# Kernel tuning notes

Measured on AMD Instinct MI355X. Metric: run time of the kernel, lower is better.

The kernel has to match this reference:

```python
import jax, jax.numpy as jnp
import numpy as np

B, S, XDIM, YDIM = 64, 1024, 256, 128


def setup_inputs() -> dict:
    key = jax.random.key(0)
    ks = jax.random.split(key, 7)
    q = jax.random.normal(ks[0], (B, S, XDIM), dtype=jnp.float32)
    # Linear weights in torch layout [out, in]; biases [out]
    sc = 1.0 / np.sqrt(XDIM)
    Wq = jax.random.normal(ks[1], (YDIM, XDIM), dtype=jnp.float32) * sc
    Wk = jax.random.normal(ks[2], (YDIM, XDIM), dtype=jnp.float32) * sc
    Wv = jax.random.normal(ks[3], (YDIM, XDIM), dtype=jnp.float32) * sc
    bq = jax.random.normal(ks[4], (YDIM,), dtype=jnp.float32) * sc
    bk = jax.random.normal(ks[5], (YDIM,), dtype=jnp.float32) * sc
    bv = jax.random.normal(ks[6], (YDIM,), dtype=jnp.float32) * sc
    return {"q": q, "Wq": Wq, "bq": bq, "Wk": Wk, "bk": bk, "Wv": Wv, "bv": bv}


def reference(q, Wq, bq, Wk, bk, Wv, bv):
    # Q, K, V projections: [B, S, YDIM]
    Q = jnp.einsum('bsx,yx->bsy', q, Wq) + bq
    K = jnp.einsum('bsx,yx->bsy', q, Wk) + bk
    V = jnp.einsum('bsx,yx->bsy', q, Wv) + bv
    scale = jnp.float32(np.sqrt(YDIM))
    # scores [B, S_q, S_k]; softmax over the QUERY axis (dim=-2), non-standard
    scores = jnp.einsum('bqd,bkd->bqk', Q, K) / scale
    attn = jax.nn.softmax(scores, axis=-2)
    out = jnp.einsum('bqk,bkd->bqd', attn, V)  # [B, S, YDIM]
    # flat=True: max over dim=-2 -> [B, YDIM]
    return jnp.max(out, axis=-2)
```

## Files before the change

### kernel.cpp

```cpp
#include <hip/hip_runtime.h>

typedef __bf16 bf16;
typedef __attribute__((ext_vector_type(8))) __bf16 bf16x8;
typedef __attribute__((ext_vector_type(4))) __bf16 bf16x4;
typedef __attribute__((ext_vector_type(4))) float  f32x4;

static __device__ __forceinline__ f32x4 mfma16(bf16x8 a, bf16x8 b, f32x4 c) {
  return __builtin_amdgcn_mfma_f32_16x16x32_bf16(a, b, c, 0, 0, 0);
}
static __device__ __forceinline__ float fexp2(float x) {
  return __builtin_amdgcn_exp2f(x);
}

#define EXP_C1 (1.4426950408889634f / 11.313708498984760f)

typedef const __attribute__((address_space(1))) unsigned int gas_u32;
typedef __attribute__((address_space(3))) unsigned int las_u32;
#define GLDS16(gp, lp) __builtin_amdgcn_global_load_lds((gas_u32*)(gp), (las_u32*)(lp), 16, 0, 0)

#define DMA_FENCE() __asm__ volatile("s_waitcnt vmcnt(0)" ::: "memory")


__global__ __launch_bounds__(256) void k_prep(
    const float* __restrict__ Wq, const float* __restrict__ Wk,
    const float* __restrict__ Wv, bf16* __restrict__ Wc)
{
  int id = blockIdx.x * 256 + threadIdx.x;
  int proj = id >> 12, r = id & 4095;
  int g = r >> 7, n = r & 127;
  const float* W = proj == 0 ? Wq : proj == 1 ? Wk : Wv;
  const float4* src = (const float4*)(W + n * 256 + g * 8);
  float4 a = src[0], b = src[1];
  bf16x8 o = { (bf16)a.x, (bf16)a.y, (bf16)a.z, (bf16)a.w,
               (bf16)b.x, (bf16)b.y, (bf16)b.z, (bf16)b.w };
  *(bf16x8*)(Wc + (size_t)proj * 32768 + g * 1024 + n * 8) = o;
}

__global__ __launch_bounds__(256, 4) void k_qkv(
    const float* __restrict__ q, const bf16* __restrict__ Wc,
    const float* __restrict__ bq, const float* __restrict__ bk, const float* __restrict__ bv,
    bf16* __restrict__ Qb, bf16* __restrict__ Kb, bf16* __restrict__ VT)
{
  __shared__ bf16 Al[32 * 520];

  const int tid = threadIdx.x, lane = tid & 63, wave = tid >> 6;
  const int ln = lane & 15, quad = lane >> 4;
  const int wc = wave;
  const int m0 = blockIdx.x * 64;

  {
    const float* src = q + (size_t)m0 * 256;
    for (int it = 0; it < 16; ++it) {
      int f = it * 1024 + tid * 4;
      int r = f >> 8, c = f & 255;
      float4 v = *(const float4*)(src + f);
      bf16x4 o = { (bf16)v.x, (bf16)v.y, (bf16)v.z, (bf16)v.w };
      *(bf16x4*)&Al[(c >> 3) * 520 + r * 8 + (c & 7)] = o;
    }
  }
  __syncthreads();

  const int b = m0 >> 10, st = (m0 & 1023) >> 7, s_off = m0 & 64;
  const size_t tbase = ((size_t)b * 8 + st) * 16384;

  for (int p = 0; p < 3; ++p) {
    const bf16* W = Wc + (size_t)p * 32768;
    const float* bias = p == 0 ? bq : p == 1 ? bk : bv;
    if (p < 2) {
      f32x4 acc[2][4] = {};
      for (int kk = 0; kk < 8; ++kk) {
        int g = kk * 4 + quad;
        bf16x8 ax[4], bw[2];
        for (int t = 0; t < 4; ++t)
          ax[t] = *(const bf16x8*)&Al[g * 520 + (t * 16 + ln) * 8];
        for (int t = 0; t < 2; ++t)
          bw[t] = *(const bf16x8*)(W + g * 1024 + (wc * 32 + t * 16 + ln) * 8);
        for (int i = 0; i < 2; ++i)
          for (int j = 0; j < 4; ++j)
            acc[i][j] = mfma16(bw[i], ax[j], acc[i][j]);
      }
      bf16* dst = (p == 0 ? Qb : Kb) + tbase;
      for (int i = 0; i < 2; ++i) {
        float4 b4 = *(const float4*)&bias[wc * 32 + i * 16 + quad * 4];
        int gd = wc * 4 + i * 2 + (quad >> 1);
        int e0 = (quad & 1) * 4;
        for (int j = 0; j < 4; ++j) {
          int s = s_off + j * 16 + ln;
          bf16x4 o = { (bf16)(acc[i][j][0] + b4.x), (bf16)(acc[i][j][1] + b4.y),
                       (bf16)(acc[i][j][2] + b4.z), (bf16)(acc[i][j][3] + b4.w) };
          *(bf16x4*)&dst[(size_t)gd * 1024 + (size_t)s * 8 + e0] = o;
        }
      }
    } else {
      f32x4 acc[4][2] = {};
      for (int kk = 0; kk < 8; ++kk) {
        int g = kk * 4 + quad;
        bf16x8 ax[4], bw[2];
        for (int t = 0; t < 4; ++t)
          ax[t] = *(const bf16x8*)&Al[g * 520 + (t * 16 + ln) * 8];
        for (int t = 0; t < 2; ++t)
          bw[t] = *(const bf16x8*)(W + g * 1024 + (wc * 32 + t * 16 + ln) * 8);
        for (int i = 0; i < 4; ++i)
          for (int j = 0; j < 2; ++j)
            acc[i][j] = mfma16(ax[i], bw[j], acc[i][j]);
      }
      bf16* dst = VT + tbase;
      for (int j = 0; j < 2; ++j) {
        int d = wc * 32 + j * 16 + ln;
        float bb = bias[d];
        for (int i = 0; i < 4; ++i) {
          int s0 = s_off + i * 16 + quad * 4;
          int G  = (s0 >> 5) * 4 + ((s0 & 15) >> 2);
          int e0 = (s0 & 16) >> 2;
          bf16x4 o = { (bf16)(acc[i][j][0] + bb), (bf16)(acc[i][j][1] + bb),
                       (bf16)(acc[i][j][2] + bb), (bf16)(acc[i][j][3] + bb) };
          *(bf16x4*)&dst[(size_t)G * 1024 + (size_t)d * 8 + e0] = o;
        }
      }
    }
  }
}

__global__ __launch_bounds__(256, 2) void k_stats(
    const bf16* __restrict__ Qb, const bf16* __restrict__ Kb, float* __restrict__ inv)
{
  __shared__ char Qbuf[2][32768];
  const int b = blockIdx.x, kt = blockIdx.y;
  const int tid = threadIdx.x, lane = tid & 63, wave = tid >> 6;
  const int ln = lane & 15, quad = lane >> 4;

  const bf16* ktile = Kb + ((size_t)b * 8 + kt) * 16384;
  bf16x8 ak[2][4];
  for (int i = 0; i < 2; ++i)
    for (int kk = 0; kk < 4; ++kk)
      ak[i][kk] = *(const bf16x8*)(ktile + (kk * 4 + quad) * 1024 + (wave * 32 + i * 16 + ln) * 8);

  const char* qb_b = (const char*)(Qb + (size_t)b * 8 * 16384);
  for (int c = 0; c < 8; ++c)
    GLDS16(qb_b + (wave * 8 + c) * 1024 + lane * 16, &Qbuf[0][(wave * 8 + c) * 1024]);

  f32x4 csum[2] = {};
  for (int qt = 0; qt < 8; ++qt) {
    DMA_FENCE();
    __syncthreads();
    if (qt < 7)
      for (int c = 0; c < 8; ++c)
        GLDS16(qb_b + (size_t)(qt + 1) * 32768 + (wave * 8 + c) * 1024 + lane * 16,
               &Qbuf[(qt + 1) & 1][(wave * 8 + c) * 1024]);
    const char* Ql = Qbuf[qt & 1];
    for (int jq = 0; jq < 8; ++jq) {
      f32x4 s0 = {}, s1 = {};
      for (int kk = 0; kk < 4; ++kk) {
        bf16x8 bqf = *(const bf16x8*)(Ql + ((kk * 4 + quad) * 2 + (jq >> 2)) * 1024
                                         + ((jq * 16 + ln) & 63) * 16);
        s0 = mfma16(ak[0][kk], bqf, s0);
        s1 = mfma16(ak[1][kk], bqf, s1);
      }
      for (int rr = 0; rr < 4; ++rr) {
        csum[0][rr] += fexp2(s0[rr] * EXP_C1);
        csum[1][rr] += fexp2(s1[rr] * EXP_C1);
      }
    }
  }
  for (int i = 0; i < 2; ++i)
    for (int rr = 0; rr < 4; ++rr) {
      float v = csum[i][rr];
      v += __shfl_xor(v, 1, 64); v += __shfl_xor(v, 2, 64);
      v += __shfl_xor(v, 4, 64); v += __shfl_xor(v, 8, 64);
      csum[i][rr] = v;
    }
  if (ln == 0) {
    float* dst = inv + (size_t)b * 1024 + kt * 128 + wave * 32 + quad * 4;
    for (int i = 0; i < 2; ++i)
      for (int rr = 0; rr < 4; ++rr)
        dst[i * 16 + rr] = 1.0f / csum[i][rr];
  }
}

__global__ __launch_bounds__(256, 2) void k_attn(
    const bf16* __restrict__ Qb, const bf16* __restrict__ Kb, const bf16* __restrict__ VT,
    const float* __restrict__ inv, float* __restrict__ Opart)
{
  __shared__ char buf[2][32768];
  __shared__ float invl[1024];
  __shared__ float redm[4][128];

  const int b = blockIdx.x, qt = blockIdx.y;
  const int tid = threadIdx.x, lane = tid & 63, wave = tid >> 6;
  const int ln = lane & 15, quad = lane >> 4;

  *(float4*)&invl[tid * 4] = *(const float4*)(inv + (size_t)b * 1024 + tid * 4);

  const bf16* qtile = Qb + ((size_t)b * 8 + qt) * 16384;
  bf16x8 bq_[2][4];
  for (int j = 0; j < 2; ++j)
    for (int kk = 0; kk < 4; ++kk)
      bq_[j][kk] = *(const bf16x8*)(qtile + (kk * 4 + quad) * 1024 + (wave * 32 + j * 16 + ln) * 8);

  const char* kb_b = (const char*)(Kb + (size_t)b * 8 * 16384);
  const char* vt_b = (const char*)(VT + (size_t)b * 8 * 16384);

#define DMA_TILE(t) do {                                                         \
    const char* ksrc = kb_b + (size_t)((t) >> 1) * 32768 + ((t) & 1) * 1024;     \
    const char* vsrc = vt_b + (size_t)((t) >> 1) * 32768 + ((t) & 1) * 16384;    \
    char* d_ = buf[(t) & 1];                                                     \
    for (int c = 0; c < 4; ++c) {                                                \
      int ch = wave * 4 + c;                                                     \
      GLDS16(ksrc + ch * 2048 + lane * 16, d_ + ch * 1024);                      \
      GLDS16(vsrc + (ch >> 1) * 2048 + (ch & 1) * 1024 + lane * 16,              \
             d_ + 16384 + ch * 1024);                                            \
    }                                                                            \
  } while (0)

  f32x4 oacc[2][8] = {};
  DMA_TILE(0);

  for (int t = 0; t < 16; ++t) {
    DMA_FENCE();
    __syncthreads();
    if (t < 15) DMA_TILE(t + 1);
    const char* Kl = buf[t & 1];
    const char* Vl = buf[t & 1] + 16384;

    f32x4 sacc[4][2] = {};
    for (int kk = 0; kk < 4; ++kk) {
      bf16x8 ak[4];
      for (int i = 0; i < 4; ++i)
        ak[i] = *(const bf16x8*)(Kl + (kk * 4 + quad) * 1024 + (i * 16 + ln) * 16);
      for (int i = 0; i < 4; ++i)
        for (int j = 0; j < 2; ++j)
          sacc[i][j] = mfma16(ak[i], bq_[j][kk], sacc[i][j]);
    }
    bf16x8 pf[2][2];
    for (int s = 0; s < 2; ++s) {
      float4 iv0 = *(float4*)&invl[t * 64 + (2 * s) * 16 + quad * 4];
      float4 iv1 = *(float4*)&invl[t * 64 + (2 * s + 1) * 16 + quad * 4];
      for (int j = 0; j < 2; ++j) {
        f32x4 lo = sacc[2 * s][j], hi = sacc[2 * s + 1][j];
        pf[j][s] = bf16x8{
          (bf16)(fexp2(lo[0] * EXP_C1) * iv0.x), (bf16)(fexp2(lo[1] * EXP_C1) * iv0.y),
          (bf16)(fexp2(lo[2] * EXP_C1) * iv0.z), (bf16)(fexp2(lo[3] * EXP_C1) * iv0.w),
          (bf16)(fexp2(hi[0] * EXP_C1) * iv1.x), (bf16)(fexp2(hi[1] * EXP_C1) * iv1.y),
          (bf16)(fexp2(hi[2] * EXP_C1) * iv1.z), (bf16)(fexp2(hi[3] * EXP_C1) * iv1.w) };
      }
    }
    for (int s = 0; s < 2; ++s)
      for (int j2 = 0; j2 < 8; ++j2) {
        bf16x8 bv_ = *(const bf16x8*)(Vl + ((s * 4 + quad) * 2 + (j2 >> 2)) * 1024
                                         + ((j2 * 16 + ln) & 63) * 16);
        oacc[0][j2] = mfma16(pf[0][s], bv_, oacc[0][j2]);
        oacc[1][j2] = mfma16(pf[1][s], bv_, oacc[1][j2]);
      }
  }

  for (int j2 = 0; j2 < 8; ++j2) {
    float m = -3.4e38f;
    for (int j = 0; j < 2; ++j)
      for (int rr = 0; rr < 4; ++rr)
        m = fmaxf(m, oacc[j][j2][rr]);
    m = fmaxf(m, __shfl_xor(m, 16, 64));
    m = fmaxf(m, __shfl_xor(m, 32, 64));
    if (lane < 16) redm[wave][j2 * 16 + ln] = m;
  }
  __syncthreads();
  if (tid < 128)
    Opart[((size_t)b * 8 + qt) * 128 + tid] =
      fmaxf(fmaxf(redm[0][tid], redm[1][tid]), fmaxf(redm[2][tid], redm[3][tid]));
}

__global__ __launch_bounds__(256) void k_final(
    const float* __restrict__ Opart, float* __restrict__ out)
{
  int t = blockIdx.x * 256 + threadIdx.x;
  int b = t >> 7, d = t & 127;
  const float* p = Opart + (size_t)b * 1024 + d;
  float m = p[0];
  for (int i = 1; i < 8; ++i) m = fmaxf(m, p[(size_t)i * 128]);
  out[t] = m;
}

extern "C" void kernel_launch(void* const* d_in, const int* in_sizes, int n_in,
                              void* d_out, int out_size, void* d_ws, size_t ws_size,
                              hipStream_t stream) {
  const float* q  = (const float*)d_in[0];
  const float* Wq = (const float*)d_in[1];
  const float* bq = (const float*)d_in[2];
  const float* Wk = (const float*)d_in[3];
  const float* bk = (const float*)d_in[4];
  const float* Wv = (const float*)d_in[5];
  const float* bv = (const float*)d_in[6];
  float* out = (float*)d_out;

  char* ws = (char*)d_ws;
  bf16*  Qb    = (bf16*)(ws);
  bf16*  Kb    = (bf16*)(ws + (16u << 20));
  bf16*  VT    = (bf16*)(ws + (32u << 20));
  float* inv   = (float*)(ws + (48u << 20));
  float* Opart = (float*)(ws + (48u << 20) + (512u << 10));
  bf16*  Wc    = (bf16*)(ws + (49u << 20));

  k_prep <<<48,           256, 0, stream>>>(Wq, Wk, Wv, Wc);
  k_qkv  <<<dim3(1024),   256, 0, stream>>>(q, Wc, bq, bk, bv, Qb, Kb, VT);
  k_stats<<<dim3(64, 8),  256, 0, stream>>>(Qb, Kb, inv);
  k_attn <<<dim3(64, 8),  256, 0, stream>>>(Qb, Kb, VT, inv, Opart);
  k_final<<<32, 256, 0, stream>>>(Opart, out);
}
```

Measured before the change: 92.57 us.

## Halve per-block tile in stats and attention kernels to double grid size

The stats and attention kernels now give each block 64 key or query rows instead of 128. Each wave owns 16 rows, and the K/V and Q streaming tiles shrink to 32 or 64 rows, so the grid grows from 512 to 1024 blocks and LDS per block halves, allowing 4 blocks per CU. The goal is more blocks and occupancy to hide latency on a GPU with many CUs. The cost is that each block reloads the full Q (stats) or K/V (attention) stream for half the work, doubling that global/L2 traffic and the barrier count per unit of work, and k_final now reduces 16 partials.

```diff
diff --git a/kernel.cpp b/kernel.cpp
--- a/kernel.cpp
+++ b/kernel.cpp
@@ -121,67 +121,64 @@
   }
 }
 
-__global__ __launch_bounds__(256, 2) void k_stats(
+__global__ __launch_bounds__(256, 4) void k_stats(
     const bf16* __restrict__ Qb, const bf16* __restrict__ Kb, float* __restrict__ inv)
 {
-  __shared__ char Qbuf[2][32768];
+  __shared__ char Qbuf[2][16384];
   const int b = blockIdx.x, kt = blockIdx.y;
   const int tid = threadIdx.x, lane = tid & 63, wave = tid >> 6;
   const int ln = lane & 15, quad = lane >> 4;
 
-  const bf16* ktile = Kb + ((size_t)b * 8 + kt) * 16384;
-  bf16x8 ak[2][4];
-  for (int i = 0; i < 2; ++i)
-    for (int kk = 0; kk < 4; ++kk)
-      ak[i][kk] = *(const bf16x8*)(ktile + (kk * 4 + quad) * 1024 + (wave * 32 + i * 16 + ln) * 8);
+  const bf16* ktile = Kb + ((size_t)b * 8 + (kt >> 1)) * 16384;
+  const int krow = (kt & 1) * 64 + wave * 16 + ln;
+  bf16x8 ak[4];
+  for (int kk = 0; kk < 4; ++kk)
+    ak[kk] = *(const bf16x8*)(ktile + (kk * 4 + quad) * 1024 + krow * 8);
 
   const char* qb_b = (const char*)(Qb + (size_t)b * 8 * 16384);
-  for (int c = 0; c < 8; ++c)
-    GLDS16(qb_b + (wave * 8 + c) * 1024 + lane * 16, &Qbuf[0][(wave * 8 + c) * 1024]);
-
-  f32x4 csum[2] = {};
-  for (int qt = 0; qt < 8; ++qt) {
+#define QDMA(c) do {                                                            \
+    char* d_ = Qbuf[(c) & 1];                                                   \
+    for (int cc = 0; cc < 4; ++cc) {                                            \
+      int ck = wave * 4 + cc;                                                   \
+      GLDS16(qb_b + (size_t)((c) >> 1) * 32768 + ck * 2048 + ((c) & 1) * 1024   \
+                  + lane * 16, d_ + ck * 1024);                                 \
+    }                                                                           \
+  } while (0)
+
+  QDMA(0);
+  f32x4 csum = {};
+  for (int c = 0; c < 16; ++c) {
     DMA_FENCE();
     __syncthreads();
-    if (qt < 7)
-      for (int c = 0; c < 8; ++c)
-        GLDS16(qb_b + (size_t)(qt + 1) * 32768 + (wave * 8 + c) * 1024 + lane * 16,
-               &Qbuf[(qt + 1) & 1][(wave * 8 + c) * 1024]);
-    const char* Ql = Qbuf[qt & 1];
-    for (int jq = 0; jq < 8; ++jq) {
-      f32x4 s0 = {}, s1 = {};
+    if (c < 15) QDMA(c + 1);
+    const char* Ql = Qbuf[c & 1];
+    for (int jq = 0; jq < 4; ++jq) {
+      f32x4 s = {};
       for (int kk = 0; kk < 4; ++kk) {
-        bf16x8 bqf = *(const bf16x8*)(Ql + ((kk * 4 + quad) * 2 + (jq >> 2)) * 1024
-                                         + ((jq * 16 + ln) & 63) * 16);
-        s0 = mfma16(ak[0][kk], bqf, s0);
-        s1 = mfma16(ak[1][kk], bqf, s1);
-      }
-      for (int rr = 0; rr < 4; ++rr) {
-        csum[0][rr] += fexp2(s0[rr] * EXP_C1);
-        csum[1][rr] += fexp2(s1[rr] * EXP_C1);
-      }
-    }
-  }
-  for (int i = 0; i < 2; ++i)
-    for (int rr = 0; rr < 4; ++rr) {
-      float v = csum[i][rr];
-      v += __shfl_xor(v, 1, 64); v += __shfl_xor(v, 2, 64);
-      v += __shfl_xor(v, 4, 64); v += __shfl_xor(v, 8, 64);
-      csum[i][rr] = v;
-    }
+        bf16x8 bqf = *(const bf16x8*)(Ql + (kk * 4 + quad) * 1024 + (jq * 16 + ln) * 16);
+        s = mfma16(ak[kk], bqf, s);
+      }
+      for (int rr = 0; rr < 4; ++rr) csum[rr] += fexp2(s[rr] * EXP_C1);
+    }
+  }
+  for (int rr = 0; rr < 4; ++rr) {
+    float v = csum[rr];
+    v += __shfl_xor(v, 1, 64); v += __shfl_xor(v, 2, 64);
+    v += __shfl_xor(v, 4, 64); v += __shfl_xor(v, 8, 64);
+    csum[rr] = v;
+  }
   if (ln == 0) {
-    float* dst = inv + (size_t)b * 1024 + kt * 128 + wave * 32 + quad * 4;
-    for (int i = 0; i < 2; ++i)
-      for (int rr = 0; rr < 4; ++rr)
-        dst[i * 16 + rr] = 1.0f / csum[i][rr];
-  }
-}
-
-__global__ __launch_bounds__(256, 2) void k_attn(
+    float* dst = inv + (size_t)b * 1024 + kt * 64 + wave * 16 + quad * 4;
+    for (int rr = 0; rr < 4; ++rr) dst[rr] = 1.0f / csum[rr];
+  }
+#undef QDMA
+}
+
+__global__ __launch_bounds__(256, 4) void k_attn(
     const bf16* __restrict__ Qb, const bf16* __restrict__ Kb, const bf16* __restrict__ VT,
     const float* __restrict__ inv, float* __restrict__ Opart)
 {
-  __shared__ char buf[2][32768];
+  __shared__ char buf[2][16384];
   __shared__ float invl[1024];
   __shared__ float redm[4][128];
 
@@ -191,80 +188,68 @@
 
   *(float4*)&invl[tid * 4] = *(const float4*)(inv + (size_t)b * 1024 + tid * 4);
 
-  const bf16* qtile = Qb + ((size_t)b * 8 + qt) * 16384;
-  bf16x8 bq_[2][4];
-  for (int j = 0; j < 2; ++j)
-    for (int kk = 0; kk < 4; ++kk)
-      bq_[j][kk] = *(const bf16x8*)(qtile + (kk * 4 + quad) * 1024 + (wave * 32 + j * 16 + ln) * 8);
+  const bf16* qtile = Qb + ((size_t)b * 8 + (qt >> 1)) * 16384;
+  const int qrow = (qt & 1) * 64 + wave * 16 + ln;
+  bf16x8 bq_[4];
+  for (int kk = 0; kk < 4; ++kk)
+    bq_[kk] = *(const bf16x8*)(qtile + (kk * 4 + quad) * 1024 + qrow * 8);
 
   const char* kb_b = (const char*)(Kb + (size_t)b * 8 * 16384);
   const char* vt_b = (const char*)(VT + (size_t)b * 8 * 16384);
 
-#define DMA_TILE(t) do {                                                         \
-    const char* ksrc = kb_b + (size_t)((t) >> 1) * 32768 + ((t) & 1) * 1024;     \
-    const char* vsrc = vt_b + (size_t)((t) >> 1) * 32768 + ((t) & 1) * 16384;    \
-    char* d_ = buf[(t) & 1];                                                     \
-    for (int c = 0; c < 4; ++c) {                                                \
-      int ch = wave * 4 + c;                                                     \
-      GLDS16(ksrc + ch * 2048 + lane * 16, d_ + ch * 1024);                      \
-      GLDS16(vsrc + (ch >> 1) * 2048 + (ch & 1) * 1024 + lane * 16,              \
-             d_ + 16384 + ch * 1024);                                            \
-    }                                                                            \
+#define DMA_TILE(t) do {                                                        \
+    const char* ksrc = kb_b + (size_t)((t) >> 2) * 32768 + ((t) & 3) * 512;     \
+    const char* vsrc = vt_b + (size_t)((t) >> 2) * 32768 + ((t) & 3) * 8192;    \
+    char* d_ = buf[(t) & 1];                                                    \
+    for (int c = 0; c < 2; ++c) {                                               \
+      int ck = wave * 2 + c;                                                    \
+      GLDS16(ksrc + (ck * 2 + (lane >> 5)) * 2048 + (lane & 31) * 16,           \
+             d_ + ck * 1024);                                                   \
+      GLDS16(vsrc + ck * 1024 + lane * 16, d_ + 8192 + ck * 1024);              \
+    }                                                                           \
   } while (0)
 
-  f32x4 oacc[2][8] = {};
+  f32x4 oacc[8] = {};
   DMA_TILE(0);
 
-  for (int t = 0; t < 16; ++t) {
+  for (int t = 0; t < 32; ++t) {
     DMA_FENCE();
     __syncthreads();
-    if (t < 15) DMA_TILE(t + 1);
+    if (t < 31) DMA_TILE(t + 1);
     const char* Kl = buf[t & 1];
-    const char* Vl = buf[t & 1] + 16384;
-
-    f32x4 sacc[4][2] = {};
+    const char* Vl = buf[t & 1] + 8192;
+
+    f32x4 sacc[2] = {};
     for (int kk = 0; kk < 4; ++kk) {
-      bf16x8 ak[4];
-      for (int i = 0; i < 4; ++i)
-        ak[i] = *(const bf16x8*)(Kl + (kk * 4 + quad) * 1024 + (i * 16 + ln) * 16);
-      for (int i = 0; i < 4; ++i)
-        for (int j = 0; j < 2; ++j)
-          sacc[i][j] = mfma16(ak[i], bq_[j][kk], sacc[i][j]);
-    }
-    bf16x8 pf[2][2];
-    for (int s = 0; s < 2; ++s) {
-      float4 iv0 = *(float4*)&invl[t * 64 + (2 * s) * 16 + quad * 4];
-      float4 iv1 = *(float4*)&invl[t * 64 + (2 * s + 1) * 16 + quad * 4];
-      for (int j = 0; j < 2; ++j) {
-        f32x4 lo = sacc[2 * s][j], hi = sacc[2 * s + 1][j];
-        pf[j][s] = bf16x8{
-          (bf16)(fexp2(lo[0] * EXP_C1) * iv0.x), (bf16)(fexp2(lo[1] * EXP_C1) * iv0.y),
-          (bf16)(fexp2(lo[2] * EXP_C1) * iv0.z), (bf16)(fexp2(lo[3] * EXP_C1) * iv0.w),
-          (bf16)(fexp2(hi[0] * EXP_C1) * iv1.x), (bf16)(fexp2(hi[1] * EXP_C1) * iv1.y),
-          (bf16)(fexp2(hi[2] * EXP_C1) * iv1.z), (bf16)(fexp2(hi[3] * EXP_C1) * iv1.w) };
-      }
-    }
-    for (int s = 0; s < 2; ++s)
-      for (int j2 = 0; j2 < 8; ++j2) {
-        bf16x8 bv_ = *(const bf16x8*)(Vl + ((s * 4 + quad) * 2 + (j2 >> 2)) * 1024
-                                         + ((j2 * 16 + ln) & 63) * 16);
-        oacc[0][j2] = mfma16(pf[0][s], bv_, oacc[0][j2]);
-        oacc[1][j2] = mfma16(pf[1][s], bv_, oacc[1][j2]);
-      }
-  }
+      bf16x8 ak0 = *(const bf16x8*)(Kl + (kk * 4 + quad) * 512 + ln * 16);
+      bf16x8 ak1 = *(const bf16x8*)(Kl + (kk * 4 + quad) * 512 + (16 + ln) * 16);
+      sacc[0] = mfma16(ak0, bq_[kk], sacc[0]);
+      sacc[1] = mfma16(ak1, bq_[kk], sacc[1]);
+    }
+    float4 iv0 = *(float4*)&invl[t * 32 + quad * 4];
+    float4 iv1 = *(float4*)&invl[t * 32 + 16 + quad * 4];
+    bf16x8 pf = {
+      (bf16)(fexp2(sacc[0][0] * EXP_C1) * iv0.x), (bf16)(fexp2(sacc[0][1] * EXP_C1) * iv0.y),
+      (bf16)(fexp2(sacc[0][2] * EXP_C1) * iv0.z), (bf16)(fexp2(sacc[0][3] * EXP_C1) * iv0.w),
+      (bf16)(fexp2(sacc[1][0] * EXP_C1) * iv1.x), (bf16)(fexp2(sacc[1][1] * EXP_C1) * iv1.y),
+      (bf16)(fexp2(sacc[1][2] * EXP_C1) * iv1.z), (bf16)(fexp2(sacc[1][3] * EXP_C1) * iv1.w) };
+    for (int j2 = 0; j2 < 8; ++j2) {
+      bf16x8 bv_ = *(const bf16x8*)(Vl + (quad * 2 + (j2 >> 2)) * 1024
+                                       + ((j2 * 16 + ln) & 63) * 16);
+      oacc[j2] = mfma16(pf, bv_, oacc[j2]);
+    }
+  }
+#undef DMA_TILE
 
   for (int j2 = 0; j2 < 8; ++j2) {
-    float m = -3.4e38f;
-    for (int j = 0; j < 2; ++j)
-      for (int rr = 0; rr < 4; ++rr)
-        m = fmaxf(m, oacc[j][j2][rr]);
+    float m = fmaxf(fmaxf(oacc[j2][0], oacc[j2][1]), fmaxf(oacc[j2][2], oacc[j2][3]));
     m = fmaxf(m, __shfl_xor(m, 16, 64));
     m = fmaxf(m, __shfl_xor(m, 32, 64));
     if (lane < 16) redm[wave][j2 * 16 + ln] = m;
   }
   __syncthreads();
   if (tid < 128)
-    Opart[((size_t)b * 8 + qt) * 128 + tid] =
+    Opart[((size_t)b * 16 + qt) * 128 + tid] =
       fmaxf(fmaxf(redm[0][tid], redm[1][tid]), fmaxf(redm[2][tid], redm[3][tid]));
 }
 
@@ -273,9 +258,9 @@
 {
   int t = blockIdx.x * 256 + threadIdx.x;
   int b = t >> 7, d = t & 127;
-  const float* p = Opart + (size_t)b * 1024 + d;
+  const float* p = Opart + (size_t)b * 2048 + d;
   float m = p[0];
-  for (int i = 1; i < 8; ++i) m = fmaxf(m, p[(size_t)i * 128]);
+  for (int i = 1; i < 16; ++i) m = fmaxf(m, p[(size_t)i * 128]);
   out[t] = m;
 }
 
@@ -296,12 +281,12 @@
   bf16*  Kb    = (bf16*)(ws + (16u << 20));
   bf16*  VT    = (bf16*)(ws + (32u << 20));
   float* inv   = (float*)(ws + (48u << 20));
-  float* Opart = (float*)(ws + (48u << 20) + (512u << 10));
+  float* Opart = (float*)(ws + (48u << 20) + (256u << 10));
   bf16*  Wc    = (bf16*)(ws + (49u << 20));
 
   k_prep <<<48,           256, 0, stream>>>(Wq, Wk, Wv, Wc);
   k_qkv  <<<dim3(1024),   256, 0, stream>>>(q, Wc, bq, bk, bv, Qb, Kb, VT);
-  k_stats<<<dim3(64, 8),  256, 0, stream>>>(Qb, Kb, inv);
-  k_attn <<<dim3(64, 8),  256, 0, stream>>>(Qb, Kb, VT, inv, Opart);
+  k_stats<<<dim3(64, 16), 256, 0, stream>>>(Qb, Kb, inv);
+  k_attn <<<dim3(64, 16), 256, 0, stream>>>(Qb, Kb, VT, inv, Opart);
   k_final<<<32, 256, 0, stream>>>(Opart, out);
 }
```

After: 103.9 us. 1.12x slower.

## Deepen LDS DMA pipeline to four smaller stages with partial vmcnt waits

Applied to the files above, without the earlier changes.

Both k_stats and k_attn switch from a double-buffered LDS pipeline with full vmcnt(0) waits to a four-slot ring of half-size tiles, prefetching three tiles ahead. Waits are relaxed to vmcnt(8)/vmcnt(4) so later loads can stay in flight while the current tile is computed. This keeps the same LDS footprint but more sync points (twice as many barriers), and the index math for K/V/Q tiles is remapped to the smaller tile shapes.

```diff
diff --git a/kernel.cpp b/kernel.cpp
--- a/kernel.cpp
+++ b/kernel.cpp
@@ -18,7 +18,7 @@
 typedef __attribute__((address_space(3))) unsigned int las_u32;
 #define GLDS16(gp, lp) __builtin_amdgcn_global_load_lds((gas_u32*)(gp), (las_u32*)(lp), 16, 0, 0)
 
-#define DMA_FENCE() __asm__ volatile("s_waitcnt vmcnt(0)" ::: "memory")
+#define WAITN(n) __asm__ volatile("s_waitcnt vmcnt(" #n ")" ::: "memory")
 
 
 __global__ __launch_bounds__(256) void k_prep(
@@ -124,7 +124,7 @@
 __global__ __launch_bounds__(256, 2) void k_stats(
     const bf16* __restrict__ Qb, const bf16* __restrict__ Kb, float* __restrict__ inv)
 {
-  __shared__ char Qbuf[2][32768];
+  __shared__ char Qbuf[4][16384];
   const int b = blockIdx.x, kt = blockIdx.y;
   const int tid = threadIdx.x, lane = tid & 63, wave = tid >> 6;
   const int ln = lane & 15, quad = lane >> 4;
@@ -136,23 +136,28 @@
       ak[i][kk] = *(const bf16x8*)(ktile + (kk * 4 + quad) * 1024 + (wave * 32 + i * 16 + ln) * 8);
 
   const char* qb_b = (const char*)(Qb + (size_t)b * 8 * 16384);
-  for (int c = 0; c < 8; ++c)
-    GLDS16(qb_b + (wave * 8 + c) * 1024 + lane * 16, &Qbuf[0][(wave * 8 + c) * 1024]);
-
+#define QDMA(c) do {                                                            \
+    char* d_ = Qbuf[(c) & 3];                                                   \
+    for (int cc = 0; cc < 4; ++cc) {                                            \
+      int ck = wave * 4 + cc;                                                   \
+      GLDS16(qb_b + (size_t)((c) >> 1) * 32768 + ck * 2048 + ((c) & 1) * 1024   \
+                  + lane * 16, d_ + ck * 1024);                                 \
+    }                                                                           \
+  } while (0)
+
+  QDMA(0); QDMA(1); QDMA(2);
   f32x4 csum[2] = {};
-  for (int qt = 0; qt < 8; ++qt) {
-    DMA_FENCE();
+  for (int c = 0; c < 16; ++c) {
+    if (c < 14)      WAITN(8);
+    else if (c == 14) WAITN(4);
+    else              WAITN(0);
     __syncthreads();
-    if (qt < 7)
-      for (int c = 0; c < 8; ++c)
-        GLDS16(qb_b + (size_t)(qt + 1) * 32768 + (wave * 8 + c) * 1024 + lane * 16,
-               &Qbuf[(qt + 1) & 1][(wave * 8 + c) * 1024]);
-    const char* Ql = Qbuf[qt & 1];
-    for (int jq = 0; jq < 8; ++jq) {
+    if (c < 13) QDMA(c + 3);
+    const char* Ql = Qbuf[c & 3];
+    for (int jq = 0; jq < 4; ++jq) {
       f32x4 s0 = {}, s1 = {};
       for (int kk = 0; kk < 4; ++kk) {
-        bf16x8 bqf = *(const bf16x8*)(Ql + ((kk * 4 + quad) * 2 + (jq >> 2)) * 1024
-                                         + ((jq * 16 + ln) & 63) * 16);
+        bf16x8 bqf = *(const bf16x8*)(Ql + (kk * 4 + quad) * 1024 + (jq * 16 + ln) * 16);
         s0 = mfma16(ak[0][kk], bqf, s0);
         s1 = mfma16(ak[1][kk], bqf, s1);
       }
@@ -162,6 +167,7 @@
       }
     }
   }
+#undef QDMA
   for (int i = 0; i < 2; ++i)
     for (int rr = 0; rr < 4; ++rr) {
       float v = csum[i][rr];
@@ -181,7 +187,7 @@
     const bf16* __restrict__ Qb, const bf16* __restrict__ Kb, const bf16* __restrict__ VT,
     const float* __restrict__ inv, float* __restrict__ Opart)
 {
-  __shared__ char buf[2][32768];
+  __shared__ char buf[4][16384];
   __shared__ float invl[1024];
   __shared__ float redm[4][128];
 
@@ -200,58 +206,58 @@
   const char* kb_b = (const char*)(Kb + (size_t)b * 8 * 16384);
   const char* vt_b = (const char*)(VT + (size_t)b * 8 * 16384);
 
-#define DMA_TILE(t) do {                                                         \
-    const char* ksrc = kb_b + (size_t)((t) >> 1) * 32768 + ((t) & 1) * 1024;     \
-    const char* vsrc = vt_b + (size_t)((t) >> 1) * 32768 + ((t) & 1) * 16384;    \
-    char* d_ = buf[(t) & 1];                                                     \
-    for (int c = 0; c < 4; ++c) {                                                \
-      int ch = wave * 4 + c;                                                     \
-      GLDS16(ksrc + ch * 2048 + lane * 16, d_ + ch * 1024);                      \
-      GLDS16(vsrc + (ch >> 1) * 2048 + (ch & 1) * 1024 + lane * 16,              \
-             d_ + 16384 + ch * 1024);                                            \
-    }                                                                            \
+#define DMA_TILE(t) do {                                                        \
+    const char* ksrc = kb_b + (size_t)((t) >> 2) * 32768 + ((t) & 3) * 512;     \
+    const char* vsrc = vt_b + (size_t)((t) >> 2) * 32768 + ((t) & 3) * 8192;    \
+    char* d_ = buf[(t) & 3];                                                    \
+    for (int c = 0; c < 2; ++c) {                                               \
+      int ck = wave * 2 + c;                                                    \
+      GLDS16(ksrc + (ck * 2 + (lane >> 5)) * 2048 + (lane & 31) * 16,           \
+             d_ + ck * 1024);                                                   \
+      GLDS16(vsrc + ck * 1024 + lane * 16, d_ + 8192 + ck * 1024);              \
+    }                                                                           \
   } while (0)
 
   f32x4 oacc[2][8] = {};
-  DMA_TILE(0);
-
-  for (int t = 0; t < 16; ++t) {
-    DMA_FENCE();
+  DMA_TILE(0); DMA_TILE(1); DMA_TILE(2);
+
+  for (int t = 0; t < 32; ++t) {
+    if (t < 30)      WAITN(8);
+    else if (t == 30) WAITN(4);
+    else              WAITN(0);
     __syncthreads();
-    if (t < 15) DMA_TILE(t + 1);
-    const char* Kl = buf[t & 1];
-    const char* Vl = buf[t & 1] + 16384;
-
-    f32x4 sacc[4][2] = {};
+    if (t < 29) DMA_TILE(t + 3);
+    const char* Kl = buf[t & 3];
+    const char* Vl = buf[t & 3] + 8192;
+
+    f32x4 sacc[2][2] = {};
     for (int kk = 0; kk < 4; ++kk) {
-      bf16x8 ak[4];
-      for (int i = 0; i < 4; ++i)
-        ak[i] = *(const bf16x8*)(Kl + (kk * 4 + quad) * 1024 + (i * 16 + ln) * 16);
-      for (int i = 0; i < 4; ++i)
-        for (int j = 0; j < 2; ++j)
-          sacc[i][j] = mfma16(ak[i], bq_[j][kk], sacc[i][j]);
-    }
-    bf16x8 pf[2][2];
-    for (int s = 0; s < 2; ++s) {
-      float4 iv0 = *(float4*)&invl[t * 64 + (2 * s) * 16 + quad * 4];
-      float4 iv1 = *(float4*)&invl[t * 64 + (2 * s + 1) * 16 + quad * 4];
+      bf16x8 ak0 = *(const bf16x8*)(Kl + (kk * 4 + quad) * 512 + ln * 16);
+      bf16x8 ak1 = *(const bf16x8*)(Kl + (kk * 4 + quad) * 512 + (16 + ln) * 16);
       for (int j = 0; j < 2; ++j) {
-        f32x4 lo = sacc[2 * s][j], hi = sacc[2 * s + 1][j];
-        pf[j][s] = bf16x8{
-          (bf16)(fexp2(lo[0] * EXP_C1) * iv0.x), (bf16)(fexp2(lo[1] * EXP_C1) * iv0.y),
-          (bf16)(fexp2(lo[2] * EXP_C1) * iv0.z), (bf16)(fexp2(lo[3] * EXP_C1) * iv0.w),
-          (bf16)(fexp2(hi[0] * EXP_C1) * iv1.x), (bf16)(fexp2(hi[1] * EXP_C1) * iv1.y),
-          (bf16)(fexp2(hi[2] * EXP_C1) * iv1.z), (bf16)(fexp2(hi[3] * EXP_C1) * iv1.w) };
-      }
-    }
-    for (int s = 0; s < 2; ++s)
-      for (int j2 = 0; j2 < 8; ++j2) {
-        bf16x8 bv_ = *(const bf16x8*)(Vl + ((s * 4 + quad) * 2 + (j2 >> 2)) * 1024
-                                         + ((j2 * 16 + ln) & 63) * 16);
-        oacc[0][j2] = mfma16(pf[0][s], bv_, oacc[0][j2]);
-        oacc[1][j2] = mfma16(pf[1][s], bv_, oacc[1][j2]);
-      }
-  }
+        sacc[0][j] = mfma16(ak0, bq_[j][kk], sacc[0][j]);
+        sacc[1][j] = mfma16(ak1, bq_[j][kk], sacc[1][j]);
+      }
+    }
+    float4 iv0 = *(float4*)&invl[t * 32 + quad * 4];
+    float4 iv1 = *(float4*)&invl[t * 32 + 16 + quad * 4];
+    bf16x8 pf[2];
+    for (int j = 0; j < 2; ++j) {
+      f32x4 lo = sacc[0][j], hi = sacc[1][j];
+      pf[j] = bf16x8{
+        (bf16)(fexp2(lo[0] * EXP_C1) * iv0.x), (bf16)(fexp2(lo[1] * EXP_C1) * iv0.y),
+        (bf16)(fexp2(lo[2] * EXP_C1) * iv0.z), (bf16)(fexp2(lo[3] * EXP_C1) * iv0.w),
+        (bf16)(fexp2(hi[0] * EXP_C1) * iv1.x), (bf16)(fexp2(hi[1] * EXP_C1) * iv1.y),
+        (bf16)(fexp2(hi[2] * EXP_C1) * iv1.z), (bf16)(fexp2(hi[3] * EXP_C1) * iv1.w) };
+    }
+    for (int j2 = 0; j2 < 8; ++j2) {
+      bf16x8 bv_ = *(const bf16x8*)(Vl + (quad * 2 + (j2 >> 2)) * 1024
+                                       + ((j2 * 16 + ln) & 63) * 16);
+      oacc[0][j2] = mfma16(pf[0], bv_, oacc[0][j2]);
+      oacc[1][j2] = mfma16(pf[1], bv_, oacc[1][j2]);
+    }
+  }
+#undef DMA_TILE
 
   for (int j2 = 0; j2 < 8; ++j2) {
     float m = -3.4e38f;
```

Measured after the change: 97.13 us. +4.9%, slower.
